# Kernel optimization log

Hardware: AMD Instinct MI355X
Metric: run time of the kernel (lower is better)

## Reference

```python
import jax, jax.numpy as jnp
import numpy as np

D_MODEL = 512
NUM_HEADS = 8
D_K = D_MODEL // NUM_HEADS
NEG_INF = -1.0e9


def setup_inputs() -> dict:
    key = jax.random.key(0)
    ks = jax.random.split(key, 8)
    B, L = 4, 2048
    q = jax.random.normal(ks[0], (B, L, D_MODEL), dtype=jnp.float32)
    k = jax.random.normal(ks[1], (B, L, D_MODEL), dtype=jnp.float32)
    v = jax.random.normal(ks[2], (B, L, D_MODEL), dtype=jnp.float32)
    mask = jax.random.randint(ks[3], (B, 1, 1, L), 0, 2, dtype=jnp.int32)
    s = 1.0 / np.sqrt(D_MODEL)
    w_q = jax.random.normal(ks[4], (D_MODEL, D_MODEL), dtype=jnp.float32) * s
    w_k = jax.random.normal(ks[5], (D_MODEL, D_MODEL), dtype=jnp.float32) * s
    w_v = jax.random.normal(ks[6], (D_MODEL, D_MODEL), dtype=jnp.float32) * s
    w_o = jax.random.normal(ks[7], (D_MODEL, D_MODEL), dtype=jnp.float32) * s
    return {"q": q, "k": k, "v": v, "mask": mask,
            "w_q": w_q, "w_k": w_k, "w_v": w_v, "w_o": w_o}


def reference(q, k, v, mask, w_q, w_k, w_v, w_o):
    B, Lq, _ = q.shape
    Lk = k.shape[1]
    # Linear projections (nn.Linear: x @ W.T); weights stored as (out,in)
    qh = (q @ w_q.T).reshape(B, Lq, NUM_HEADS, D_K).transpose(0, 2, 1, 3)
    kh = (k @ w_k.T).reshape(B, Lk, NUM_HEADS, D_K).transpose(0, 2, 1, 3)
    vh = (v @ w_v.T).reshape(B, Lk, NUM_HEADS, D_K).transpose(0, 2, 1, 3)
    scale = 1.0 / np.sqrt(D_K)
    scores = jnp.einsum('bhqd,bhkd->bhqk', qh, kh) * scale  # (B,H,Lq,Lk)
    scores = jnp.where(mask == 0, jnp.float32(NEG_INF), scores)
    attn = jax.nn.softmax(scores, axis=-1)
    # dropout is identity in eval mode
    x = jnp.einsum('bhqk,bhkd->bhqd', attn, vh)
    x = x.transpose(0, 2, 1, 3).reshape(B, Lq, D_MODEL)
    return x @ w_o.T
```

## Files before the change

kernel.cpp:

```cpp
#include <hip/hip_runtime.h>

#define D_MODEL 512
#define NHEAD 8
#define DK 64
#define SEQ 2048
#define NEG_INF -1.0e9f

typedef __attribute__((ext_vector_type(8))) short bf16x8;
typedef __attribute__((ext_vector_type(4))) float f32x4;

__device__ __forceinline__ unsigned short f2bf_rne(float x) {
  union { float f; unsigned u; } v; v.f = x;
  return (unsigned short)((v.u + 0x7FFFu + ((v.u >> 16) & 1u)) >> 16);
}
__device__ __forceinline__ float bf2f(unsigned short b) {
  union { unsigned u; float f; } v; v.u = ((unsigned)b) << 16;
  return v.f;
}
__device__ __forceinline__ void split_rne(float x, unsigned short& hi,
                                          unsigned short& lo) {
  hi = f2bf_rne(x);
  lo = f2bf_rne(x - bf2f(hi));
}
__device__ __forceinline__ void split_trunc(float x, unsigned short& hi,
                                            unsigned short& lo) {
  union { float f; unsigned u; } v; v.f = x;
  hi = (unsigned short)(v.u >> 16);
  union { float f; unsigned u; } r; r.f = x - bf2f(hi);
  lo = (unsigned short)(r.u >> 16);
}

__device__ __forceinline__ void gload_lds16(const void* g, void* l) {
  __builtin_amdgcn_global_load_lds(
      (const __attribute__((address_space(1))) unsigned int*)g,
      (__attribute__((address_space(3))) unsigned int*)l, 16, 0, 0);
}

__global__ __launch_bounds__(256) void split_tile(const float* __restrict__ A,
                                                  unsigned short* __restrict__ Xh,
                                                  unsigned short* __restrict__ Xl) {
  const int e = blockIdx.x * 256 + threadIdx.x;
  const int m = e >> 7;
  const int c0 = (e & 127) << 2;
  const float4 a = *(const float4*)(A + (size_t)m * 512 + c0);
  ushort4 h4, l4;
  split_rne(a.x, h4.x, l4.x);
  split_rne(a.y, h4.y, l4.y);
  split_rne(a.z, h4.z, l4.z);
  split_rne(a.w, h4.w, l4.w);
  const int r = m & 63, mt = m >> 6, kt = c0 >> 6, cc = c0 & 63;
  const int off = (mt * 8 + kt) * 4096 + r * 64 + (cc ^ ((r & 7) << 3));
  *(ushort4*)&Xh[off] = h4;
  *(ushort4*)&Xl[off] = l4;
}

#define EPI_Q 0
#define EPI_K 1
#define EPI_VT 2
#define EPI_OUT 3

template <int EPI>
__global__ __launch_bounds__(256) void gemm_split(
    const unsigned short* __restrict__ Ah, const unsigned short* __restrict__ Al,
    const float* __restrict__ W,
    unsigned short* __restrict__ Ch, unsigned short* __restrict__ Cl,
    float* __restrict__ Cf) {
  __shared__ unsigned short Ash[4096], Asl[4096], Wsh[4096], Wsl[4096];
  const int tid = threadIdx.x;
  const int w = tid >> 6, lane = tid & 63, lg = lane >> 4, lc = lane & 15;
  const int mt = blockIdx.x, nt = blockIdx.y;

  f32x4 acc[4] = {{0, 0, 0, 0}, {0, 0, 0, 0}, {0, 0, 0, 0}, {0, 0, 0, 0}};

  const int wr = tid >> 2;
  const int wc0 = (tid & 3) << 4;
  const float* Wrow = W + (size_t)(nt * 64 + wr) * 512;

  for (int kt = 0; kt < 8; ++kt) {
    const size_t tb = (size_t)(mt * 8 + kt) * 4096;
    const unsigned short* sh = Ah + tb + w * 512 + lane * 8;
    const unsigned short* sl = Al + tb + w * 512 + lane * 8;
    gload_lds16(sh, &Ash[w * 512]);
    gload_lds16(sh + 2048, &Ash[w * 512 + 2048]);
    gload_lds16(sl, &Asl[w * 512]);
    gload_lds16(sl + 2048, &Asl[w * 512 + 2048]);
#pragma unroll
    for (int j = 0; j < 4; ++j) {
      const float4 wv = *(const float4*)(Wrow + kt * 64 + wc0 + j * 4);
      ushort4 h4, l4;
      split_trunc(wv.x, h4.x, l4.x);
      split_trunc(wv.y, h4.y, l4.y);
      split_trunc(wv.z, h4.z, l4.z);
      split_trunc(wv.w, h4.w, l4.w);
      const int off = wr * 64 + ((wc0 + j * 4) ^ ((wr & 7) << 3));
      *(ushort4*)&Wsh[off] = h4;
      *(ushort4*)&Wsl[off] = l4;
    }
    __syncthreads();
#pragma unroll
    for (int s = 0; s < 2; ++s) {
      const int arow = w * 16 + lc;
      const int aoff = arow * 64 + ((s * 32 + lg * 8) ^ ((arow & 7) << 3));
      const bf16x8 a_hi = *(const bf16x8*)&Ash[aoff];
      const bf16x8 a_lo = *(const bf16x8*)&Asl[aoff];
#pragma unroll
      for (int ct = 0; ct < 4; ++ct) {
        const int brow = ct * 16 + lc;
        const int boff = brow * 64 + ((s * 32 + lg * 8) ^ ((brow & 7) << 3));
        const bf16x8 b_hi = *(const bf16x8*)&Wsh[boff];
        const bf16x8 b_lo = *(const bf16x8*)&Wsl[boff];
        acc[ct] = __builtin_amdgcn_mfma_f32_16x16x32_bf16(a_hi, b_hi, acc[ct], 0, 0, 0);
        acc[ct] = __builtin_amdgcn_mfma_f32_16x16x32_bf16(a_hi, b_lo, acc[ct], 0, 0, 0);
        acc[ct] = __builtin_amdgcn_mfma_f32_16x16x32_bf16(a_lo, b_hi, acc[ct], 0, 0, 0);
      }
    }
    __syncthreads();
  }

#pragma unroll
  for (int ct = 0; ct < 4; ++ct) {
#pragma unroll
    for (int reg = 0; reg < 4; ++reg) {
      const float val = acc[ct][reg];
      const int row = w * 16 + lg * 4 + reg;
      const int m = mt * 64 + row;
      const int col = ct * 16 + lc;
      if (EPI == EPI_OUT) {
        Cf[(size_t)m * 512 + nt * 64 + col] = val;
      } else {
        unsigned short hi, lo;
        split_rne(val, hi, lo);
        const int b = m >> 11, l = m & 2047;
        if (EPI == EPI_Q) {
          const size_t o = ((size_t)(b * 8 + nt) * 2048 + l) * 64 + col;
          Ch[o] = hi; Cl[o] = lo;
        } else if (EPI == EPI_K) {
          const int kti = l >> 6, r = l & 63;
          const size_t o = ((size_t)((b * 8 + nt) * 32 + kti)) * 4096 +
                           r * 64 + (col ^ ((r & 7) << 3));
          Ch[o] = hi; Cl[o] = lo;
        } else {
          const int kti = l >> 6, key = l & 63;
          const size_t o = ((size_t)((b * 8 + nt) * 32 + kti)) * 4096 +
                           col * 64 + (key ^ ((col & 7) << 3));
          Ch[o] = hi; Cl[o] = lo;
        }
      }
    }
  }
}

__global__ __launch_bounds__(256) void attn_fwd_mfma(
    const unsigned short* __restrict__ qhh, const unsigned short* __restrict__ qhl,
    const unsigned short* __restrict__ khh, const unsigned short* __restrict__ khl,
    const unsigned short* __restrict__ vth, const unsigned short* __restrict__ vtl,
    const int* __restrict__ mask,
    unsigned short* __restrict__ xh, unsigned short* __restrict__ xl) {
  __shared__ unsigned short Ksh_h[4096], Ksh_l[4096];
  __shared__ unsigned short Vts_h[4096], Vts_l[4096];
  __shared__ unsigned short Ps_h[4096], Ps_l[4096];
  __shared__ int Ms[64];

  const int tid = threadIdx.x;
  const int w = tid >> 6, lane = tid & 63, lg = lane >> 4, lc = lane & 15;
  const int qt = blockIdx.x, h = blockIdx.y, b = blockIdx.z;

  const size_t qbase = ((size_t)(b * 8 + h) * 2048 + qt * 64 + w * 16 + lc) * 64;
  bf16x8 qa_hi[2], qa_lo[2];
#pragma unroll
  for (int s = 0; s < 2; ++s) {
    qa_hi[s] = *(const bf16x8*)(qhh + qbase + s * 32 + lg * 8);
    qa_lo[s] = *(const bf16x8*)(qhl + qbase + s * 32 + lg * 8);
  }

  float m_run[4] = {-1e30f, -1e30f, -1e30f, -1e30f};
  float l_run[4] = {0.f, 0.f, 0.f, 0.f};
  f32x4 o_acc[4] = {{0, 0, 0, 0}, {0, 0, 0, 0}, {0, 0, 0, 0}, {0, 0, 0, 0}};
  const float scale = 0.125f;

  for (int kt = 0; kt < 32; ++kt) {
    const size_t tb = ((size_t)((b * 8 + h) * 32 + kt)) * 4096;
    const int so = w * 512 + lane * 8;
    gload_lds16(khh + tb + so, &Ksh_h[w * 512]);
    gload_lds16(khh + tb + so + 2048, &Ksh_h[w * 512 + 2048]);
    gload_lds16(khl + tb + so, &Ksh_l[w * 512]);
    gload_lds16(khl + tb + so + 2048, &Ksh_l[w * 512 + 2048]);
    gload_lds16(vth + tb + so, &Vts_h[w * 512]);
    gload_lds16(vth + tb + so + 2048, &Vts_h[w * 512 + 2048]);
    gload_lds16(vtl + tb + so, &Vts_l[w * 512]);
    gload_lds16(vtl + tb + so + 2048, &Vts_l[w * 512 + 2048]);
    if (tid < 64) Ms[tid] = mask[b * SEQ + kt * 64 + tid];
    __syncthreads();

    f32x4 s_acc[4];
#pragma unroll
    for (int ct = 0; ct < 4; ++ct) {
      f32x4 acc = {0, 0, 0, 0};
#pragma unroll
      for (int s = 0; s < 2; ++s) {
        const int row = ct * 16 + lc;
        const int off = row * 64 + ((s * 32 + lg * 8) ^ ((row & 7) << 3));
        const bf16x8 kb_hi = *(const bf16x8*)&Ksh_h[off];
        const bf16x8 kb_lo = *(const bf16x8*)&Ksh_l[off];
        acc = __builtin_amdgcn_mfma_f32_16x16x32_bf16(qa_hi[s], kb_hi, acc, 0, 0, 0);
        acc = __builtin_amdgcn_mfma_f32_16x16x32_bf16(qa_hi[s], kb_lo, acc, 0, 0, 0);
        acc = __builtin_amdgcn_mfma_f32_16x16x32_bf16(qa_lo[s], kb_hi, acc, 0, 0, 0);
      }
      s_acc[ct] = acc;
    }

    float p_val[4][4];
    int mv[4];
#pragma unroll
    for (int ct = 0; ct < 4; ++ct) mv[ct] = Ms[ct * 16 + lc];
#pragma unroll
    for (int reg = 0; reg < 4; ++reg) {
      const float s0 = mv[0] ? s_acc[0][reg] * scale : NEG_INF;
      const float s1 = mv[1] ? s_acc[1][reg] * scale : NEG_INF;
      const float s2 = mv[2] ? s_acc[2][reg] * scale : NEG_INF;
      const float s3 = mv[3] ? s_acc[3][reg] * scale : NEG_INF;
      float rmax = fmaxf(fmaxf(s0, s1), fmaxf(s2, s3));
      rmax = fmaxf(rmax, __shfl_xor(rmax, 1));
      rmax = fmaxf(rmax, __shfl_xor(rmax, 2));
      rmax = fmaxf(rmax, __shfl_xor(rmax, 4));
      rmax = fmaxf(rmax, __shfl_xor(rmax, 8));
      const float mnew = fmaxf(m_run[reg], rmax);
      const float alpha = __expf(m_run[reg] - mnew);
      m_run[reg] = mnew;
      const float p0 = __expf(s0 - mnew), p1 = __expf(s1 - mnew);
      const float p2 = __expf(s2 - mnew), p3 = __expf(s3 - mnew);
      float rsum = p0 + p1 + p2 + p3;
      rsum += __shfl_xor(rsum, 1);
      rsum += __shfl_xor(rsum, 2);
      rsum += __shfl_xor(rsum, 4);
      rsum += __shfl_xor(rsum, 8);
      l_run[reg] = l_run[reg] * alpha + rsum;
      p_val[0][reg] = p0; p_val[1][reg] = p1;
      p_val[2][reg] = p2; p_val[3][reg] = p3;
#pragma unroll
      for (int dt = 0; dt < 4; ++dt) o_acc[dt][reg] *= alpha;
    }

#pragma unroll
    for (int ct = 0; ct < 4; ++ct)
#pragma unroll
      for (int reg = 0; reg < 4; ++reg) {
        const int row = w * 16 + lg * 4 + reg;
        const int col = ct * 16 + lc;
        unsigned short hi, lo;
        split_trunc(p_val[ct][reg], hi, lo);
        const int off = row * 64 + (col ^ ((row & 7) << 3));
        Ps_h[off] = hi;
        Ps_l[off] = lo;
      }

#pragma unroll
    for (int s = 0; s < 2; ++s) {
      const int arow = w * 16 + lc;
      const int aoff = arow * 64 + ((s * 32 + lg * 8) ^ ((arow & 7) << 3));
      const bf16x8 pa_hi = *(const bf16x8*)&Ps_h[aoff];
      const bf16x8 pa_lo = *(const bf16x8*)&Ps_l[aoff];
#pragma unroll
      for (int dt = 0; dt < 4; ++dt) {
        const int brow = dt * 16 + lc;
        const int boff = brow * 64 + ((s * 32 + lg * 8) ^ ((brow & 7) << 3));
        const bf16x8 vb_hi = *(const bf16x8*)&Vts_h[boff];
        const bf16x8 vb_lo = *(const bf16x8*)&Vts_l[boff];
        o_acc[dt] = __builtin_amdgcn_mfma_f32_16x16x32_bf16(pa_hi, vb_hi, o_acc[dt], 0, 0, 0);
        o_acc[dt] = __builtin_amdgcn_mfma_f32_16x16x32_bf16(pa_hi, vb_lo, o_acc[dt], 0, 0, 0);
        o_acc[dt] = __builtin_amdgcn_mfma_f32_16x16x32_bf16(pa_lo, vb_hi, o_acc[dt], 0, 0, 0);
      }
    }
    __syncthreads();
  }

#pragma unroll
  for (int reg = 0; reg < 4; ++reg) {
    const float inv = 1.0f / l_run[reg];
    const int row = w * 16 + lg * 4 + reg;
    const size_t tbase = ((size_t)((b * 32 + qt) * 8 + h)) * 4096;
#pragma unroll
    for (int dt = 0; dt < 4; ++dt) {
      const int c = dt * 16 + lc;
      unsigned short hi, lo;
      split_rne(o_acc[dt][reg] * inv, hi, lo);
      const size_t o = tbase + row * 64 + (c ^ ((row & 7) << 3));
      xh[o] = hi;
      xl[o] = lo;
    }
  }
}

extern "C" void kernel_launch(void* const* d_in, const int* in_sizes, int n_in,
                              void* d_out, int out_size, void* d_ws,
                              size_t ws_size, hipStream_t stream) {
  const float* q = (const float*)d_in[0];
  const float* k = (const float*)d_in[1];
  const float* v = (const float*)d_in[2];
  const int* mask = (const int*)d_in[3];
  const float* w_q = (const float*)d_in[4];
  const float* w_k = (const float*)d_in[5];
  const float* w_v = (const float*)d_in[6];
  const float* w_o = (const float*)d_in[7];
  float* out = (float*)d_out;

  unsigned short* ws = (unsigned short*)d_ws;
  const size_t SZ = 4194304;
  unsigned short* Xh = ws;
  unsigned short* Xl = ws + SZ;
  unsigned short* qh_h = ws + 2 * SZ; unsigned short* qh_l = ws + 3 * SZ;
  unsigned short* kh_h = ws + 4 * SZ; unsigned short* kh_l = ws + 5 * SZ;
  unsigned short* vt_h = ws + 6 * SZ; unsigned short* vt_l = ws + 7 * SZ;

  dim3 blk(256);
  dim3 gs(4096);
  dim3 gg(128, 8);
  dim3 ga(32, 8, 4);

  split_tile<<<gs, blk, 0, stream>>>(q, Xh, Xl);
  gemm_split<EPI_Q><<<gg, blk, 0, stream>>>(Xh, Xl, w_q, qh_h, qh_l, nullptr);
  split_tile<<<gs, blk, 0, stream>>>(k, Xh, Xl);
  gemm_split<EPI_K><<<gg, blk, 0, stream>>>(Xh, Xl, w_k, kh_h, kh_l, nullptr);
  split_tile<<<gs, blk, 0, stream>>>(v, Xh, Xl);
  gemm_split<EPI_VT><<<gg, blk, 0, stream>>>(Xh, Xl, w_v, vt_h, vt_l, nullptr);
  attn_fwd_mfma<<<ga, blk, 0, stream>>>(qh_h, qh_l, kh_h, kh_l, vt_h, vt_l,
                                        mask, Xh, Xl);
  gemm_split<EPI_OUT><<<gg, blk, 0, stream>>>(Xh, Xl, w_o, nullptr, nullptr, out);
}
```

Baseline: 379.2 us.

## Double-buffer K/V and GEMM tiles, use exp2 softmax with lazy rescale

The attention kernel now double-buffers K/V tiles in LDS and prefetches the next tile while computing the current one. It reads the mask directly per lane instead of staging it in LDS, and drops the trailing barrier. Softmax works in the exp2 domain with pre-scaled constants, and the running-max rescale of accumulators is skipped when no row's max grows. The projection GEMM doubles its M tile to 128 rows, double-buffers A tiles, prefetches W into registers one k-step ahead, and raises wave priority around the MFMA blocks. The larger LDS footprint may reduce how many blocks fit per CU.

```diff
diff --git a/kernel.cpp b/kernel.cpp
--- a/kernel.cpp
+++ b/kernel.cpp
@@ -4,7 +4,9 @@
 #define NHEAD 8
 #define DK 64
 #define SEQ 2048
-#define NEG_INF -1.0e9f
+
+#define SCL2 0.18033688011112042f
+#define MASKL2 -1.4426950408889634e9f
 
 typedef __attribute__((ext_vector_type(8))) short bf16x8;
 typedef __attribute__((ext_vector_type(4))) float f32x4;
@@ -65,85 +67,112 @@
     const float* __restrict__ W,
     unsigned short* __restrict__ Ch, unsigned short* __restrict__ Cl,
     float* __restrict__ Cf) {
-  __shared__ unsigned short Ash[4096], Asl[4096], Wsh[4096], Wsl[4096];
+  __shared__ unsigned short Ash[2][8192], Asl[2][8192];
+  __shared__ unsigned short Wsh[4096], Wsl[4096];
   const int tid = threadIdx.x;
   const int w = tid >> 6, lane = tid & 63, lg = lane >> 4, lc = lane & 15;
   const int mt = blockIdx.x, nt = blockIdx.y;
 
-  f32x4 acc[4] = {{0, 0, 0, 0}, {0, 0, 0, 0}, {0, 0, 0, 0}, {0, 0, 0, 0}};
+  f32x4 acc[2][4] = {};
 
   const int wr = tid >> 2;
   const int wc0 = (tid & 3) << 4;
   const float* Wrow = W + (size_t)(nt * 64 + wr) * 512;
 
+  float4 wreg[4];
+#pragma unroll
+  for (int j = 0; j < 4; ++j)
+    wreg[j] = *(const float4*)(Wrow + wc0 + j * 4);
+
+  auto issueA = [&](int kt, int buf) {
+#pragma unroll
+    for (int sub = 0; sub < 2; ++sub) {
+      const size_t tb = ((size_t)((2 * mt + sub) * 8 + kt)) * 4096;
+      const unsigned short* sh = Ah + tb + w * 512 + lane * 8;
+      const unsigned short* sl = Al + tb + w * 512 + lane * 8;
+      gload_lds16(sh, &Ash[buf][sub * 4096 + w * 512]);
+      gload_lds16(sh + 2048, &Ash[buf][sub * 4096 + w * 512 + 2048]);
+      gload_lds16(sl, &Asl[buf][sub * 4096 + w * 512]);
+      gload_lds16(sl + 2048, &Asl[buf][sub * 4096 + w * 512 + 2048]);
+    }
+  };
+  issueA(0, 0);
+
   for (int kt = 0; kt < 8; ++kt) {
-    const size_t tb = (size_t)(mt * 8 + kt) * 4096;
-    const unsigned short* sh = Ah + tb + w * 512 + lane * 8;
-    const unsigned short* sl = Al + tb + w * 512 + lane * 8;
-    gload_lds16(sh, &Ash[w * 512]);
-    gload_lds16(sh + 2048, &Ash[w * 512 + 2048]);
-    gload_lds16(sl, &Asl[w * 512]);
-    gload_lds16(sl + 2048, &Asl[w * 512 + 2048]);
+    const int cur = kt & 1;
+    __syncthreads();
 #pragma unroll
     for (int j = 0; j < 4; ++j) {
-      const float4 wv = *(const float4*)(Wrow + kt * 64 + wc0 + j * 4);
       ushort4 h4, l4;
-      split_trunc(wv.x, h4.x, l4.x);
-      split_trunc(wv.y, h4.y, l4.y);
-      split_trunc(wv.z, h4.z, l4.z);
-      split_trunc(wv.w, h4.w, l4.w);
+      split_trunc(wreg[j].x, h4.x, l4.x);
+      split_trunc(wreg[j].y, h4.y, l4.y);
+      split_trunc(wreg[j].z, h4.z, l4.z);
+      split_trunc(wreg[j].w, h4.w, l4.w);
       const int off = wr * 64 + ((wc0 + j * 4) ^ ((wr & 7) << 3));
       *(ushort4*)&Wsh[off] = h4;
       *(ushort4*)&Wsl[off] = l4;
     }
     __syncthreads();
-#pragma unroll
-    for (int s = 0; s < 2; ++s) {
+    if (kt < 7) {
+      issueA(kt + 1, cur ^ 1);
+#pragma unroll
+      for (int j = 0; j < 4; ++j)
+        wreg[j] = *(const float4*)(Wrow + (kt + 1) * 64 + wc0 + j * 4);
+    }
+    __builtin_amdgcn_s_setprio(1);
+#pragma unroll
+    for (int ar = 0; ar < 2; ++ar) {
       const int arow = w * 16 + lc;
-      const int aoff = arow * 64 + ((s * 32 + lg * 8) ^ ((arow & 7) << 3));
-      const bf16x8 a_hi = *(const bf16x8*)&Ash[aoff];
-      const bf16x8 a_lo = *(const bf16x8*)&Asl[aoff];
-#pragma unroll
-      for (int ct = 0; ct < 4; ++ct) {
-        const int brow = ct * 16 + lc;
-        const int boff = brow * 64 + ((s * 32 + lg * 8) ^ ((brow & 7) << 3));
-        const bf16x8 b_hi = *(const bf16x8*)&Wsh[boff];
-        const bf16x8 b_lo = *(const bf16x8*)&Wsl[boff];
-        acc[ct] = __builtin_amdgcn_mfma_f32_16x16x32_bf16(a_hi, b_hi, acc[ct], 0, 0, 0);
-        acc[ct] = __builtin_amdgcn_mfma_f32_16x16x32_bf16(a_hi, b_lo, acc[ct], 0, 0, 0);
-        acc[ct] = __builtin_amdgcn_mfma_f32_16x16x32_bf16(a_lo, b_hi, acc[ct], 0, 0, 0);
-      }
-    }
-    __syncthreads();
-  }
-
-#pragma unroll
-  for (int ct = 0; ct < 4; ++ct) {
-#pragma unroll
-    for (int reg = 0; reg < 4; ++reg) {
-      const float val = acc[ct][reg];
-      const int row = w * 16 + lg * 4 + reg;
-      const int m = mt * 64 + row;
-      const int col = ct * 16 + lc;
-      if (EPI == EPI_OUT) {
-        Cf[(size_t)m * 512 + nt * 64 + col] = val;
-      } else {
-        unsigned short hi, lo;
-        split_rne(val, hi, lo);
-        const int b = m >> 11, l = m & 2047;
-        if (EPI == EPI_Q) {
-          const size_t o = ((size_t)(b * 8 + nt) * 2048 + l) * 64 + col;
-          Ch[o] = hi; Cl[o] = lo;
-        } else if (EPI == EPI_K) {
-          const int kti = l >> 6, r = l & 63;
-          const size_t o = ((size_t)((b * 8 + nt) * 32 + kti)) * 4096 +
-                           r * 64 + (col ^ ((r & 7) << 3));
-          Ch[o] = hi; Cl[o] = lo;
+      const int abase = ar * 4096 + arow * 64;
+#pragma unroll
+      for (int s = 0; s < 2; ++s) {
+        const int aoff = abase + ((s * 32 + lg * 8) ^ ((arow & 7) << 3));
+        const bf16x8 a_hi = *(const bf16x8*)&Ash[cur][aoff];
+        const bf16x8 a_lo = *(const bf16x8*)&Asl[cur][aoff];
+#pragma unroll
+        for (int ct = 0; ct < 4; ++ct) {
+          const int brow = ct * 16 + lc;
+          const int boff = brow * 64 + ((s * 32 + lg * 8) ^ ((brow & 7) << 3));
+          const bf16x8 b_hi = *(const bf16x8*)&Wsh[boff];
+          const bf16x8 b_lo = *(const bf16x8*)&Wsl[boff];
+          acc[ar][ct] = __builtin_amdgcn_mfma_f32_16x16x32_bf16(a_hi, b_hi, acc[ar][ct], 0, 0, 0);
+          acc[ar][ct] = __builtin_amdgcn_mfma_f32_16x16x32_bf16(a_hi, b_lo, acc[ar][ct], 0, 0, 0);
+          acc[ar][ct] = __builtin_amdgcn_mfma_f32_16x16x32_bf16(a_lo, b_hi, acc[ar][ct], 0, 0, 0);
+        }
+      }
+    }
+    __builtin_amdgcn_s_setprio(0);
+  }
+
+#pragma unroll
+  for (int ar = 0; ar < 2; ++ar) {
+#pragma unroll
+    for (int ct = 0; ct < 4; ++ct) {
+#pragma unroll
+      for (int reg = 0; reg < 4; ++reg) {
+        const float val = acc[ar][ct][reg];
+        const int m = mt * 128 + ar * 64 + w * 16 + lg * 4 + reg;
+        const int col = ct * 16 + lc;
+        if (EPI == EPI_OUT) {
+          Cf[(size_t)m * 512 + nt * 64 + col] = val;
         } else {
-          const int kti = l >> 6, key = l & 63;
-          const size_t o = ((size_t)((b * 8 + nt) * 32 + kti)) * 4096 +
-                           col * 64 + (key ^ ((col & 7) << 3));
-          Ch[o] = hi; Cl[o] = lo;
+          unsigned short hi, lo;
+          split_rne(val, hi, lo);
+          const int b = m >> 11, l = m & 2047;
+          if (EPI == EPI_Q) {
+            const size_t o = ((size_t)(b * 8 + nt) * 2048 + l) * 64 + col;
+            Ch[o] = hi; Cl[o] = lo;
+          } else if (EPI == EPI_K) {
+            const int kti = l >> 6, r = l & 63;
+            const size_t o = ((size_t)((b * 8 + nt) * 32 + kti)) * 4096 +
+                             r * 64 + (col ^ ((r & 7) << 3));
+            Ch[o] = hi; Cl[o] = lo;
+          } else {
+            const int kti = l >> 6, key = l & 63;
+            const size_t o = ((size_t)((b * 8 + nt) * 32 + kti)) * 4096 +
+                             col * 64 + (key ^ ((col & 7) << 3));
+            Ch[o] = hi; Cl[o] = lo;
+          }
         }
       }
     }
@@ -156,15 +185,16 @@
     const unsigned short* __restrict__ vth, const unsigned short* __restrict__ vtl,
     const int* __restrict__ mask,
     unsigned short* __restrict__ xh, unsigned short* __restrict__ xl) {
-  __shared__ unsigned short Ksh_h[4096], Ksh_l[4096];
-  __shared__ unsigned short Vts_h[4096], Vts_l[4096];
+  __shared__ unsigned short Ksh_h[2][4096], Ksh_l[2][4096];
+  __shared__ unsigned short Vts_h[2][4096], Vts_l[2][4096];
   __shared__ unsigned short Ps_h[4096], Ps_l[4096];
-  __shared__ int Ms[64];
 
   const int tid = threadIdx.x;
   const int w = tid >> 6, lane = tid & 63, lg = lane >> 4, lc = lane & 15;
   const int qt = blockIdx.x, h = blockIdx.y, b = blockIdx.z;
 
+  const size_t kvbase = (size_t)((b * 8 + h) * 32) * 4096;
+
   const size_t qbase = ((size_t)(b * 8 + h) * 2048 + qt * 64 + w * 16 + lc) * 64;
   bf16x8 qa_hi[2], qa_lo[2];
 #pragma unroll
@@ -173,72 +203,98 @@
     qa_lo[s] = *(const bf16x8*)(qhl + qbase + s * 32 + lg * 8);
   }
 
+  auto issueKV = [&](int kt, int buf) {
+    const size_t tb = kvbase + (size_t)kt * 4096;
+    const int so = w * 512 + lane * 8;
+    gload_lds16(khh + tb + so, &Ksh_h[buf][w * 512]);
+    gload_lds16(khh + tb + so + 2048, &Ksh_h[buf][w * 512 + 2048]);
+    gload_lds16(khl + tb + so, &Ksh_l[buf][w * 512]);
+    gload_lds16(khl + tb + so + 2048, &Ksh_l[buf][w * 512 + 2048]);
+    gload_lds16(vth + tb + so, &Vts_h[buf][w * 512]);
+    gload_lds16(vth + tb + so + 2048, &Vts_h[buf][w * 512 + 2048]);
+    gload_lds16(vtl + tb + so, &Vts_l[buf][w * 512]);
+    gload_lds16(vtl + tb + so + 2048, &Vts_l[buf][w * 512 + 2048]);
+  };
+  issueKV(0, 0);
+
   float m_run[4] = {-1e30f, -1e30f, -1e30f, -1e30f};
   float l_run[4] = {0.f, 0.f, 0.f, 0.f};
   f32x4 o_acc[4] = {{0, 0, 0, 0}, {0, 0, 0, 0}, {0, 0, 0, 0}, {0, 0, 0, 0}};
-  const float scale = 0.125f;
 
   for (int kt = 0; kt < 32; ++kt) {
-    const size_t tb = ((size_t)((b * 8 + h) * 32 + kt)) * 4096;
-    const int so = w * 512 + lane * 8;
-    gload_lds16(khh + tb + so, &Ksh_h[w * 512]);
-    gload_lds16(khh + tb + so + 2048, &Ksh_h[w * 512 + 2048]);
-    gload_lds16(khl + tb + so, &Ksh_l[w * 512]);
-    gload_lds16(khl + tb + so + 2048, &Ksh_l[w * 512 + 2048]);
-    gload_lds16(vth + tb + so, &Vts_h[w * 512]);
-    gload_lds16(vth + tb + so + 2048, &Vts_h[w * 512 + 2048]);
-    gload_lds16(vtl + tb + so, &Vts_l[w * 512]);
-    gload_lds16(vtl + tb + so + 2048, &Vts_l[w * 512 + 2048]);
-    if (tid < 64) Ms[tid] = mask[b * SEQ + kt * 64 + tid];
+    const int cur = kt & 1;
     __syncthreads();
+    if (kt < 31) issueKV(kt + 1, cur ^ 1);
+    int mv[4];
+#pragma unroll
+    for (int ct = 0; ct < 4; ++ct)
+      mv[ct] = mask[b * SEQ + kt * 64 + ct * 16 + lc];
 
     f32x4 s_acc[4];
+    __builtin_amdgcn_s_setprio(1);
 #pragma unroll
     for (int ct = 0; ct < 4; ++ct) {
-      f32x4 acc = {0, 0, 0, 0};
+      f32x4 a2 = {0, 0, 0, 0};
 #pragma unroll
       for (int s = 0; s < 2; ++s) {
         const int row = ct * 16 + lc;
         const int off = row * 64 + ((s * 32 + lg * 8) ^ ((row & 7) << 3));
-        const bf16x8 kb_hi = *(const bf16x8*)&Ksh_h[off];
-        const bf16x8 kb_lo = *(const bf16x8*)&Ksh_l[off];
-        acc = __builtin_amdgcn_mfma_f32_16x16x32_bf16(qa_hi[s], kb_hi, acc, 0, 0, 0);
-        acc = __builtin_amdgcn_mfma_f32_16x16x32_bf16(qa_hi[s], kb_lo, acc, 0, 0, 0);
-        acc = __builtin_amdgcn_mfma_f32_16x16x32_bf16(qa_lo[s], kb_hi, acc, 0, 0, 0);
-      }
-      s_acc[ct] = acc;
-    }
-
+        const bf16x8 kb_hi = *(const bf16x8*)&Ksh_h[cur][off];
+        const bf16x8 kb_lo = *(const bf16x8*)&Ksh_l[cur][off];
+        a2 = __builtin_amdgcn_mfma_f32_16x16x32_bf16(qa_hi[s], kb_hi, a2, 0, 0, 0);
+        a2 = __builtin_amdgcn_mfma_f32_16x16x32_bf16(qa_hi[s], kb_lo, a2, 0, 0, 0);
+        a2 = __builtin_amdgcn_mfma_f32_16x16x32_bf16(qa_lo[s], kb_hi, a2, 0, 0, 0);
+      }
+      s_acc[ct] = a2;
+    }
+    __builtin_amdgcn_s_setprio(0);
+
+    float sc[4][4];
+#pragma unroll
+    for (int ct = 0; ct < 4; ++ct) {
+      const bool dead = (mv[ct] == 0);
+#pragma unroll
+      for (int reg = 0; reg < 4; ++reg)
+        sc[ct][reg] = dead ? MASKL2 : s_acc[ct][reg] * SCL2;
+    }
+    float rmax[4];
+#pragma unroll
+    for (int reg = 0; reg < 4; ++reg) {
+      float r = fmaxf(fmaxf(sc[0][reg], sc[1][reg]), fmaxf(sc[2][reg], sc[3][reg]));
+      r = fmaxf(r, __shfl_xor(r, 1));
+      r = fmaxf(r, __shfl_xor(r, 2));
+      r = fmaxf(r, __shfl_xor(r, 4));
+      r = fmaxf(r, __shfl_xor(r, 8));
+      rmax[reg] = r;
+    }
+    const bool nonew = (rmax[0] <= m_run[0]) && (rmax[1] <= m_run[1]) &&
+                       (rmax[2] <= m_run[2]) && (rmax[3] <= m_run[3]);
+    if (!__all(nonew)) {
+#pragma unroll
+      for (int reg = 0; reg < 4; ++reg) {
+        const float mnew = fmaxf(m_run[reg], rmax[reg]);
+        const float alpha = __builtin_exp2f(m_run[reg] - mnew);
+        m_run[reg] = mnew;
+        l_run[reg] *= alpha;
+#pragma unroll
+        for (int dt = 0; dt < 4; ++dt) o_acc[dt][reg] *= alpha;
+      }
+    }
     float p_val[4][4];
-    int mv[4];
-#pragma unroll
-    for (int ct = 0; ct < 4; ++ct) mv[ct] = Ms[ct * 16 + lc];
 #pragma unroll
     for (int reg = 0; reg < 4; ++reg) {
-      const float s0 = mv[0] ? s_acc[0][reg] * scale : NEG_INF;
-      const float s1 = mv[1] ? s_acc[1][reg] * scale : NEG_INF;
-      const float s2 = mv[2] ? s_acc[2][reg] * scale : NEG_INF;
-      const float s3 = mv[3] ? s_acc[3][reg] * scale : NEG_INF;
-      float rmax = fmaxf(fmaxf(s0, s1), fmaxf(s2, s3));
-      rmax = fmaxf(rmax, __shfl_xor(rmax, 1));
-      rmax = fmaxf(rmax, __shfl_xor(rmax, 2));
-      rmax = fmaxf(rmax, __shfl_xor(rmax, 4));
-      rmax = fmaxf(rmax, __shfl_xor(rmax, 8));
-      const float mnew = fmaxf(m_run[reg], rmax);
-      const float alpha = __expf(m_run[reg] - mnew);
-      m_run[reg] = mnew;
-      const float p0 = __expf(s0 - mnew), p1 = __expf(s1 - mnew);
-      const float p2 = __expf(s2 - mnew), p3 = __expf(s3 - mnew);
-      float rsum = p0 + p1 + p2 + p3;
+      float rsum = 0.f;
+#pragma unroll
+      for (int ct = 0; ct < 4; ++ct) {
+        const float p = __builtin_exp2f(sc[ct][reg] - m_run[reg]);
+        p_val[ct][reg] = p;
+        rsum += p;
+      }
       rsum += __shfl_xor(rsum, 1);
       rsum += __shfl_xor(rsum, 2);
       rsum += __shfl_xor(rsum, 4);
       rsum += __shfl_xor(rsum, 8);
-      l_run[reg] = l_run[reg] * alpha + rsum;
-      p_val[0][reg] = p0; p_val[1][reg] = p1;
-      p_val[2][reg] = p2; p_val[3][reg] = p3;
-#pragma unroll
-      for (int dt = 0; dt < 4; ++dt) o_acc[dt][reg] *= alpha;
+      l_run[reg] += rsum;
     }
 
 #pragma unroll
@@ -254,6 +310,7 @@
         Ps_l[off] = lo;
       }
 
+    __builtin_amdgcn_s_setprio(1);
 #pragma unroll
     for (int s = 0; s < 2; ++s) {
       const int arow = w * 16 + lc;
@@ -264,14 +321,14 @@
       for (int dt = 0; dt < 4; ++dt) {
         const int brow = dt * 16 + lc;
         const int boff = brow * 64 + ((s * 32 + lg * 8) ^ ((brow & 7) << 3));
-        const bf16x8 vb_hi = *(const bf16x8*)&Vts_h[boff];
-        const bf16x8 vb_lo = *(const bf16x8*)&Vts_l[boff];
+        const bf16x8 vb_hi = *(const bf16x8*)&Vts_h[cur][boff];
+        const bf16x8 vb_lo = *(const bf16x8*)&Vts_l[cur][boff];
         o_acc[dt] = __builtin_amdgcn_mfma_f32_16x16x32_bf16(pa_hi, vb_hi, o_acc[dt], 0, 0, 0);
         o_acc[dt] = __builtin_amdgcn_mfma_f32_16x16x32_bf16(pa_hi, vb_lo, o_acc[dt], 0, 0, 0);
         o_acc[dt] = __builtin_amdgcn_mfma_f32_16x16x32_bf16(pa_lo, vb_hi, o_acc[dt], 0, 0, 0);
       }
     }
-    __syncthreads();
+    __builtin_amdgcn_s_setprio(0);
   }
 
 #pragma unroll
@@ -314,7 +371,7 @@
 
   dim3 blk(256);
   dim3 gs(4096);
-  dim3 gg(128, 8);
+  dim3 gg(64, 8);
   dim3 ga(32, 8, 4);
 
   split_tile<<<gs, blk, 0, stream>>>(q, Xh, Xl);
```

Measured after the change: 387.0 us. +2.1%, slower.
